# Kernel tuning notes

Measured on AMD Instinct MI355X. Metric: run time of the kernel, lower is better.

Reference implementation:

```python
import jax, jax.numpy as jnp
import numpy as np

SHIFT = 1  # shift_direction fixed to +1 (original picks +/-1 randomly at init)

def setup_inputs() -> dict:
    key = jax.random.key(0)
    k1, k2, k3 = jax.random.split(key, 3)
    x = jax.random.normal(k1, (1, 64, 56, 56), dtype=jnp.float32)
    w1 = jax.random.normal(k2, (64, 2), dtype=jnp.float32)      # weights[0]
    w2 = jax.random.normal(k3, (64, 64, 3), dtype=jnp.float32)  # weights[1]
    return {"x": x, "w1": w1, "w2": w2}

def reference(x, w1, w2):
    # x viewed as (1, 3584, 56, 1) with 3584 = 64*56; unfold with kernel (3,1),
    # padding (1,0) slides a size-3 window over the last 56-dim of x.
    xp = jnp.pad(x, ((0, 0), (0, 0), (0, 0), (1, 1)))            # (1,64,56,58)
    # t3[l,j,n,k,m] = x_pad[l,j,n,m+k]  -> (1,64,56,3,56), the im2col buffer
    t3 = jnp.stack([xp[..., k:k + 56] for k in range(3)], axis=3)
    # contraction over channel j and kernel tap k: a 1D conv across channels
    t4 = jnp.einsum('ljnkm,ijk->linm', t3, w2)                   # (1,64,56,56)
    # channel expand by outer product with w1
    t5 = jnp.einsum('kiml,ij->kimjl', t4, w1)                    # (1,64,56,2,56)
    # shifted-window rolls + fold + sum
    t6 = jnp.roll(t5, SHIFT, axis=2)
    t6 = t6.reshape(1, 64, 112, 56)
    t6 = jnp.roll(t6, SHIFT, axis=2)
    t6 = t6.reshape(1, 64, 56, 2, 56)
    return jnp.sum(t6, axis=3)                                   # (1,64,56,56)
```

## Files before the change

### kernel.cpp

```cpp
#include <hip/hip_runtime.h>

#define CH 64
#define NN 56
#define RPB 14
#define TR  16
#define XSTRIDE (NN*NN)

__global__ __launch_bounds__(1024, 1) void fused_shift_conv(
    const float* __restrict__ x,
    const float* __restrict__ w1,
    const float* __restrict__ w2,
    float* __restrict__ out)
{
    __shared__ float w2s[CH * 3];
    __shared__ float t4s[TR][NN];

    const int i  = blockIdx.x >> 2;
    const int g  = blockIdx.x & 3;
    const int r0 = g * RPB;

    const int tid = threadIdx.x;
    if (tid < CH * 3) w2s[tid] = w2[i * CH * 3 + tid];
    __syncthreads();

    const int wv = tid >> 6;
    const int m  = tid & 63;

    const int n = (r0 - 2 + wv + NN) % NN;

    const bool actC = (m < NN);
    const bool actL = (m >= 1) && actC;
    const bool actH = (m + 1 < NN);

    const int ml = actL ? (m - 1) : 0;
    const int mc = actC ? m       : 0;
    const int mh = actH ? (m + 1) : 0;

    const float* xrow = x + n * NN;

    float acc = 0.f;
    #pragma unroll 8
    for (int j = 0; j < CH; ++j) {
        const float* xr = xrow + j * XSTRIDE;
        float xl = xr[ml]; xl = actL ? xl : 0.f;
        float xc = xr[mc]; xc = actC ? xc : 0.f;
        float xh = xr[mh]; xh = actH ? xh : 0.f;
        acc = fmaf(xl, w2s[j*3+0], acc);
        acc = fmaf(xc, w2s[j*3+1], acc);
        acc = fmaf(xh, w2s[j*3+2], acc);
    }

    if (actC) t4s[wv][m] = acc;
    __syncthreads();

    if (wv < RPB && actC) {
        const float a0 = w1[i*2+0];
        const float a1 = w1[i*2+1];
        const float v  = fmaf(a0, t4s[wv+1][m], a1 * t4s[wv][m]);
        out[i * XSTRIDE + (r0 + wv) * NN + m] = v;
    }
}

extern "C" void kernel_launch(void* const* d_in, const int* in_sizes, int n_in,
                              void* d_out, int out_size, void* d_ws, size_t ws_size,
                              hipStream_t stream) {
    const float* x  = (const float*)d_in[0];
    const float* w1 = (const float*)d_in[1];
    const float* w2 = (const float*)d_in[2];
    float* out      = (float*)d_out;

    dim3 grid(256);
    dim3 block(1024);
    hipLaunchKernelGGL(fused_shift_conv, grid, block, 0, stream, x, w1, w2, out);
}
```

Baseline: 67.08 us.

## Use float2 loads with lane shuffles for halo and smaller blocks

```diff
diff --git a/kernel.cpp b/kernel.cpp
--- a/kernel.cpp
+++ b/kernel.cpp
@@ -2,62 +2,68 @@
 
 #define CH 64
 #define NN 56
-#define RPB 14
-#define TR  16
-#define XSTRIDE (NN*NN)
+#define XS (NN*NN)
+#define RPB 7
+#define TR  8
 
-__global__ __launch_bounds__(1024, 1) void fused_shift_conv(
+__global__ __launch_bounds__(256) void fused_shift_conv2(
     const float* __restrict__ x,
-    const float* __restrict__ w1,
-    const float* __restrict__ w2,
+    const float* __restrict__ g1,
+    const float* __restrict__ g2,
     float* __restrict__ out)
 {
-    __shared__ float w2s[CH * 3];
     __shared__ float t4s[TR][NN];
 
-    const int i  = blockIdx.x >> 2;
-    const int g  = blockIdx.x & 3;
+    const int i  = blockIdx.x >> 3;
+    const int g  = blockIdx.x & 7;
     const int r0 = g * RPB;
 
     const int tid = threadIdx.x;
-    if (tid < CH * 3) w2s[tid] = w2[i * CH * 3 + tid];
+    const int wv  = tid >> 5;
+    const int lr  = tid & 31;
+    const int n   = (r0 - 2 + wv + NN) % NN;
+
+    const bool act = (lr < 28);
+    const int  c   = (act ? lr : 27) * 2;
+
+    const bool mL = (lr == 0);
+    const bool mH = (lr == 27);
+
+    const float* xp = x + n * NN + c;
+    const float* wp = g2 + i * (CH * 3);
+
+    float accx = 0.f, accy = 0.f;
+
+    #pragma unroll 8
+    for (int j = 0; j < CH; ++j) {
+        float2 v = *(const float2*)(xp + j * XS);
+        float xl = __shfl_up(v.y, 1);
+        float xh = __shfl_down(v.x, 1);
+        xl = mL ? 0.f : xl;
+        xh = mH ? 0.f : xh;
+        const float w0 = wp[3*j+0];
+        const float w1 = wp[3*j+1];
+        const float w2 = wp[3*j+2];
+        accx = fmaf(xl,  w0, accx);
+        accx = fmaf(v.x, w1, accx);
+        accx = fmaf(v.y, w2, accx);
+        accy = fmaf(v.x, w0, accy);
+        accy = fmaf(v.y, w1, accy);
+        accy = fmaf(xh,  w2, accy);
+    }
+
+    if (act) *(float2*)&t4s[wv][c] = make_float2(accx, accy);
     __syncthreads();
 
-    const int wv = tid >> 6;
-    const int m  = tid & 63;
-
-    const int n = (r0 - 2 + wv + NN) % NN;
-
-    const bool actC = (m < NN);
-    const bool actL = (m >= 1) && actC;
-    const bool actH = (m + 1 < NN);
-
-    const int ml = actL ? (m - 1) : 0;
-    const int mc = actC ? m       : 0;
-    const int mh = actH ? (m + 1) : 0;
-
-    const float* xrow = x + n * NN;
-
-    float acc = 0.f;
-    #pragma unroll 8
-    for (int j = 0; j < CH; ++j) {
-        const float* xr = xrow + j * XSTRIDE;
-        float xl = xr[ml]; xl = actL ? xl : 0.f;
-        float xc = xr[mc]; xc = actC ? xc : 0.f;
-        float xh = xr[mh]; xh = actH ? xh : 0.f;
-        acc = fmaf(xl, w2s[j*3+0], acc);
-        acc = fmaf(xc, w2s[j*3+1], acc);
-        acc = fmaf(xh, w2s[j*3+2], acc);
-    }
-
-    if (actC) t4s[wv][m] = acc;
-    __syncthreads();
-
-    if (wv < RPB && actC) {
-        const float a0 = w1[i*2+0];
-        const float a1 = w1[i*2+1];
-        const float v  = fmaf(a0, t4s[wv+1][m], a1 * t4s[wv][m]);
-        out[i * XSTRIDE + (r0 + wv) * NN + m] = v;
+    if (wv < RPB && act) {
+        const float a0 = g1[i*2+0];
+        const float a1 = g1[i*2+1];
+        const float2 tA = *(const float2*)&t4s[wv+1][c];
+        const float2 tB = *(const float2*)&t4s[wv][c];
+        float2 o;
+        o.x = fmaf(a0, tA.x, a1 * tB.x);
+        o.y = fmaf(a0, tA.y, a1 * tB.y);
+        *(float2*)&out[i*XS + (r0 + wv)*NN + c] = o;
     }
 }
 
@@ -69,7 +75,7 @@
     const float* w2 = (const float*)d_in[2];
     float* out      = (float*)d_out;
 
-    dim3 grid(256);
-    dim3 block(1024);
-    hipLaunchKernelGGL(fused_shift_conv, grid, block, 0, stream, x, w1, w2, out);
+    dim3 grid(64 * 8);
+    dim3 block(256);
+    hipLaunchKernelGGL(fused_shift_conv2, grid, block, 0, stream, x, w1, w2, out);
 }
```

New measurement: 62.60 us. -6.7%, faster.
